# Performance work log

Hardware: AMD Instinct MI355X
Metric: run time of the kernel (lower is better)

The kernel has to match this reference:

```python
import jax, jax.numpy as jnp
import numpy as np

B, C, H, W = 32, 64, 64, 64
K = 512  # n_embeddings
D = 64   # embedding_dim


def setup_inputs() -> dict:
    key = jax.random.key(0)
    k1, k2 = jax.random.split(key)
    inputs = jax.random.normal(k1, (B, C, H, W), dtype=jnp.float32)
    embedding = jax.random.normal(k2, (K, D), dtype=jnp.float32)
    weight = jnp.ones((K,), dtype=jnp.float32)
    return {"inputs": inputs, "embedding": embedding, "weight": weight}


def reference(inputs, embedding, weight):
    # NCHW -> NHWC, flatten to [N, D]
    x = jnp.transpose(inputs, (0, 2, 3, 1))  # [B,H,W,D]
    input_shape = x.shape
    flat = x.reshape(-1, D)                  # [N,D], N = B*H*W
    n = flat.shape[0]

    usage = jnp.sum(weight >= 0.01)

    # squared Euclidean distances (argmin-equivalent to torch.cdist)
    d2 = (jnp.sum(flat * flat, axis=1, keepdims=True)
          - 2.0 * (flat @ embedding.T)
          + jnp.sum(embedding * embedding, axis=1))  # [N,K]
    indices = jnp.argmin(d2, axis=1)                 # [N]

    # one-hot assignment stats (scatter -> bincount form)
    counts = jnp.zeros((K,), dtype=flat.dtype).at[indices].add(1.0)
    avg_probs = counts / n
    perplexity = jnp.exp(-jnp.sum(avg_probs * jnp.log(avg_probs + 1e-10)))

    # straight-through quantization
    q = embedding[indices].reshape(input_shape)      # [B,H,W,D]
    quantized = jax.lax.stop_gradient(q) + x - jax.lax.stop_gradient(x)

    commitment_loss = jnp.mean((jax.lax.stop_gradient(quantized) - x) ** 2)

    quantized_nchw = jnp.transpose(quantized, (0, 3, 1, 2))
    return quantized_nchw, commitment_loss, perplexity, usage, indices
```

## Files before the change

### kernel.cpp

```cpp
#include <hip/hip_runtime.h>


typedef __attribute__((ext_vector_type(8))) _Float16 f16x8;
typedef __attribute__((ext_vector_type(4))) float f32x4;
typedef unsigned int uint;
typedef unsigned short ushort;

namespace {
constexpr int kC = 64, kH = 64, kW = 64;
constexpr int kK = 512, kD = 64;
constexpr int kHW = kH * kW;
constexpr int kCHW = kC * kHW;
constexpr int kN = 32 * kHW;
constexpr int kQElems = 32 * kC * kHW;
constexpr uint kGapFP = 21u;
}

__device__ __forceinline__ ushort hb(_Float16 h) { return __builtin_bit_cast(ushort, h); }
__device__ __forceinline__ uint umin(uint a, uint b) { return a < b ? a : b; }
__device__ __forceinline__ uint umax(uint a, uint b) { return a > b ? a : b; }

__device__ __forceinline__ void gld16(const void* g, void* l) {
  __builtin_amdgcn_global_load_lds(
      (const __attribute__((address_space(1))) uint*)g,
      (__attribute__((address_space(3))) uint*)l, 16, 0, 0);
}

__global__ __launch_bounds__(64) void vq_prep(const float* __restrict__ emb,
                                              ushort* __restrict__ embPh,
                                              ushort* __restrict__ embPl,
                                              float* __restrict__ embT,
                                              float* __restrict__ enorm,
                                              uint* __restrict__ counts,
                                              uint* __restrict__ flag_count) {
  const int k = blockIdx.x * 64 + threadIdx.x;
  const float4* __restrict__ ep4 = (const float4*)(emb + k * kD);
  float ev[kD];
  uint uh[32], ul[32];
  float s = 0.f;
#pragma unroll
  for (int j = 0; j < kD / 4; ++j) {
    const float4 v = ep4[j];
    ev[4 * j] = v.x; ev[4 * j + 1] = v.y; ev[4 * j + 2] = v.z; ev[4 * j + 3] = v.w;
    s = fmaf(v.x, v.x, s); s = fmaf(v.y, v.y, s);
    s = fmaf(v.z, v.z, s); s = fmaf(v.w, v.w, s);
#pragma unroll
    for (int t = 0; t < 2; ++t) {
      const float e0 = ev[4 * j + 2 * t] * 2048.f;
      const float e1 = ev[4 * j + 2 * t + 1] * 2048.f;
      const _Float16 h0 = (_Float16)e0, h1 = (_Float16)e1;
      const _Float16 l0 = (_Float16)(e0 - (float)h0);
      const _Float16 l1 = (_Float16)(e1 - (float)h1);
      uh[2 * j + t] = (uint)hb(h0) | ((uint)hb(h1) << 16);
      ul[2 * j + t] = (uint)hb(l0) | ((uint)hb(l1) << 16);
    }
  }
  uint4* __restrict__ ph4 = (uint4*)embPh;
  uint4* __restrict__ pl4 = (uint4*)embPl;
#pragma unroll
  for (int cc = 0; cc < 8; ++cc) {
    const int dst = k * 8 + (cc ^ (k & 7));
    ph4[dst] = uint4{uh[4 * cc], uh[4 * cc + 1], uh[4 * cc + 2], uh[4 * cc + 3]};
    pl4[dst] = uint4{ul[4 * cc], ul[4 * cc + 1], ul[4 * cc + 2], ul[4 * cc + 3]};
  }
#pragma unroll
  for (int c = 0; c < kD; ++c) embT[c * kK + k] = ev[c];
  enorm[k] = s;
  counts[k] = 0u;
  if (k == 0) *flag_count = 0u;
}

__global__ __launch_bounds__(512, 4) void vq_assign(
    const float* __restrict__ in, const ushort* __restrict__ embPh,
    const ushort* __restrict__ embPl, const float* __restrict__ embT,
    const float* __restrict__ enorm, float* __restrict__ idx_out,
    float* __restrict__ outq, uint* __restrict__ counts,
    float* __restrict__ partial, uint* __restrict__ flag_count,
    uint* __restrict__ flags, uint flag_cap) {
  __shared__ __align__(16) ushort xbh[128 * 64];
  __shared__ __align__(16) ushort xbl[128 * 64];
  __shared__ __align__(16) ushort ebh[2][4096];
  __shared__ __align__(16) ushort ebl[2][4096];
  __shared__ uint mm1[4][128], mm2[4][128];
  __shared__ float xnp[4][128];
  __shared__ uint hist[512];
  __shared__ uint fidx[128];

  const int tid = threadIdx.x;
  const int lane = tid & 63;
  const int wv = __builtin_amdgcn_readfirstlane(tid >> 6);
  const int ph = wv >> 2;
  const int cs = wv & 3;
  const int c = lane & 15;
  const int g = lane >> 4;

  const int blk = blockIdx.x;
  const int bb = blk >> 5;
  const int hw0 = (blk & 31) << 7;
  const float* __restrict__ xp = in + (size_t)bb * kCHW + hw0 + ph * 64;

  hist[tid] = 0u;

  auto stageE = [&](int buf, int st) {
    const size_t src = (size_t)st * 8192 + cs * 2048;
    const int dst = cs * 2048;
#pragma unroll
    for (int i = 0; i < 2; ++i) {
      gld16((const char*)embPh + src + i * 1024 + lane * 16,
            (char*)&ebh[buf][0] + dst + i * 1024);
      gld16((const char*)embPl + src + i * 1024 + lane * 16,
            (char*)&ebl[buf][0] + dst + i * 1024);
    }
  };
  stageE(0, 0);

  float en_pre[8];
#pragma unroll
  for (int st = 0; st < 8; ++st)
    en_pre[st] = (enorm[st * 64 + cs * 16 + c] + 256.f) * 2048.f;

  {
    const int p = lane;
    uint uh[8], ul[8];
    float xn = 0.f;
#pragma unroll
    for (int j = 0; j < 8; ++j) {
      const float f0 = xp[(size_t)(cs * 16 + 2 * j) * kHW + p];
      const float f1 = xp[(size_t)(cs * 16 + 2 * j + 1) * kHW + p];
      xn = fmaf(f0, f0, xn);
      xn = fmaf(f1, f1, xn);
      const float m0 = -2.f * f0, m1f = -2.f * f1;
      const _Float16 h0 = (_Float16)m0, h1 = (_Float16)m1f;
      const _Float16 l0 = (_Float16)(m0 - (float)h0);
      const _Float16 l1 = (_Float16)(m1f - (float)h1);
      uh[j] = (uint)hb(h0) | ((uint)hb(h1) << 16);
      ul[j] = (uint)hb(l0) | ((uint)hb(l1) << 16);
    }
    const int row = ph * 64 + p;
    const int swz = (row & 7) << 4;
    const int o0 = (row * 128 + cs * 32) ^ swz;
    const int o1 = (row * 128 + cs * 32 + 16) ^ swz;
    *(uint4*)((char*)xbh + o0) = uint4{uh[0], uh[1], uh[2], uh[3]};
    *(uint4*)((char*)xbh + o1) = uint4{uh[4], uh[5], uh[6], uh[7]};
    *(uint4*)((char*)xbl + o0) = uint4{ul[0], ul[1], ul[2], ul[3]};
    *(uint4*)((char*)xbl + o1) = uint4{ul[4], ul[5], ul[6], ul[7]};
    xnp[cs][row] = xn;
  }
  __syncthreads();

  uint m1[16], m2[16];
#pragma unroll
  for (int i = 0; i < 16; ++i) { m1[i] = 0xFFFFFFFFu; m2[i] = 0xFFFFFFFFu; }

#pragma unroll
  for (int st = 0; st < 8; ++st) {
    if (st < 7) stageE((st & 1) ^ 1, st + 1);

    if (st < 7) {
      asm volatile("s_waitcnt vmcnt(4)" ::: "memory");
    } else {
      asm volatile("s_waitcnt vmcnt(0)" ::: "memory");
    }
    __builtin_amdgcn_sched_barrier(0);

    const int rowb = cs * 16 + c;
    const int swb = (rowb & 7) << 4;
    const int ob0 = (rowb * 128 + g * 16) ^ swb;
    const int ob1 = (rowb * 128 + g * 16 + 64) ^ swb;
    const int bsel = st & 1;
    const f16x8 bh0 = *(const f16x8*)((const char*)&ebh[bsel][0] + ob0);
    const f16x8 bh1 = *(const f16x8*)((const char*)&ebh[bsel][0] + ob1);
    const f16x8 bl0 = *(const f16x8*)((const char*)&ebl[bsel][0] + ob0);
    const f16x8 bl1 = *(const f16x8*)((const char*)&ebl[bsel][0] + ob1);
    const float en = en_pre[st];
    const uint kor = (uint)(st * 64 + cs * 16 + c);
    __builtin_amdgcn_s_setprio(1);
#pragma unroll
    for (int rt = 0; rt < 4; ++rt) {
      f16x8 ah[2], al[2];
#pragma unroll
      for (int s = 0; s < 2; ++s) {
        const int row = ph * 64 + rt * 16 + c;
        const int off = (row * 128 + g * 16 + s * 64) ^ ((row & 7) << 4);
        ah[s] = *(const f16x8*)((const char*)xbh + off);
        al[s] = *(const f16x8*)((const char*)xbl + off);
      }
      f32x4 acc0 = {en, en, en, en};
      f32x4 acc1 = {0.f, 0.f, 0.f, 0.f};
      acc0 = __builtin_amdgcn_mfma_f32_16x16x32_f16(ah[0], bh0, acc0, 0, 0, 0);
      acc1 = __builtin_amdgcn_mfma_f32_16x16x32_f16(ah[1], bh1, acc1, 0, 0, 0);
      acc0 = __builtin_amdgcn_mfma_f32_16x16x32_f16(ah[0], bl0, acc0, 0, 0, 0);
      acc1 = __builtin_amdgcn_mfma_f32_16x16x32_f16(ah[1], bl1, acc1, 0, 0, 0);
      acc0 = __builtin_amdgcn_mfma_f32_16x16x32_f16(al[0], bh0, acc0, 0, 0, 0);
      acc1 = __builtin_amdgcn_mfma_f32_16x16x32_f16(al[1], bh1, acc1, 0, 0, 0);
#pragma unroll
      for (int r = 0; r < 4; ++r) {
        const uint u = ((uint)(acc0[r] + acc1[r]) << 9) | kor;
        const int i = rt * 4 + r;
        const uint t = umax(m1[i], u);
        m1[i] = umin(m1[i], u);
        m2[i] = umin(m2[i], t);
      }
    }
    __builtin_amdgcn_s_setprio(0);

    asm volatile("s_waitcnt lgkmcnt(0)" ::: "memory");
    __builtin_amdgcn_sched_barrier(0);
    __builtin_amdgcn_s_barrier();
  }

#pragma unroll
  for (int i = 0; i < 16; ++i) {
    uint a1 = m1[i], a2 = m2[i];
#pragma unroll
    for (int off = 1; off < 16; off <<= 1) {
      const uint o1 = __shfl_xor(a1, off, 64);
      const uint o2 = __shfl_xor(a2, off, 64);
      const uint t = umax(a1, o1);
      a1 = umin(a1, o1);
      a2 = umin(umin(a2, o2), t);
    }
    m1[i] = a1; m2[i] = a2;
  }

  if (c == 0) {
#pragma unroll
    for (int i = 0; i < 16; ++i) {
      const int p = ph * 64 + (i >> 2) * 16 + g * 4 + (i & 3);
      mm1[cs][p] = m1[i];
      mm2[cs][p] = m2[i];
    }
  }
  __syncthreads();

  if (tid < 128) {
    uint a1 = mm1[0][tid], a2 = mm2[0][tid];
#pragma unroll
    for (int s = 1; s < 4; ++s) {
      const uint u1 = mm1[s][tid], u2 = mm2[s][tid];
      const uint t = umax(a1, u1);
      a1 = umin(a1, u1);
      a2 = umin(umin(a2, u2), t);
    }
    const uint bidx = a1 & 511u;
    fidx[tid] = bidx;
    idx_out[blk * 128 + tid] = (float)bidx;
    if (((a2 >> 9) - (a1 >> 9)) < kGapFP) {
      const uint slot = atomicAdd(flag_count, 1u);
      if (slot < flag_cap) flags[slot] = (uint)(blk * 128 + tid);
    }
    atomicAdd(&hist[bidx], 1u);

    const float xnorm = (xnp[0][tid] + xnp[1][tid]) + (xnp[2][tid] + xnp[3][tid]);
    float d2 = fmaf((float)(a1 >> 9), 1.f / 2048.f, -256.f) + xnorm;
#pragma unroll
    for (int off = 32; off > 0; off >>= 1) d2 += __shfl_down(d2, off, 64);
    if ((tid & 63) == 0) partial[blk * 2 + (tid >> 6)] = d2;
  }
  __syncthreads();
  if (hist[tid]) atomicAdd(&counts[tid], hist[tid]);

  {
    const int ch = tid >> 3;
    const int wq = tid & 7;
    const float* __restrict__ tr = embT + ch * kK;
    float* __restrict__ oq = outq + (size_t)bb * kCHW + (size_t)ch * kHW + hw0 + wq * 16;
#pragma unroll
    for (int i = 0; i < 4; ++i) {
      const int p0 = wq * 16 + i * 4;
      float4 v;
      v.x = tr[fidx[p0 + 0]];
      v.y = tr[fidx[p0 + 1]];
      v.z = tr[fidx[p0 + 2]];
      v.w = tr[fidx[p0 + 3]];
      *(float4*)(oq + i * 4) = v;
    }
  }
}

__global__ __launch_bounds__(256) void vq_refine(const float* __restrict__ in,
                                                 const float* __restrict__ emb,
                                                 const uint* __restrict__ flag_count,
                                                 const uint* __restrict__ flags,
                                                 uint flag_cap,
                                                 float* __restrict__ idx_out,
                                                 float* __restrict__ outq) {
  uint cnt = *flag_count;
  if (cnt > flag_cap) cnt = flag_cap;
  const int lane = threadIdx.x & 63;
  const uint wave_id = blockIdx.x * 4u + (threadIdx.x >> 6);
  const uint wave_stride = gridDim.x * 4u;

  for (uint i = wave_id; i < cnt; i += wave_stride) {
    const int n = (int)flags[i];
    const int b = n >> 12;
    const int hw = n & 4095;
    const float* __restrict__ xp = in + (size_t)b * kCHW + hw;

    float xr[kD];
#pragma unroll
    for (int d = 0; d < kD; ++d) xr[d] = xp[(size_t)d * kHW];

    double best = 1e300;
    int bidx = 0;
#pragma unroll 1
    for (int kk = 0; kk < 8; ++kk) {
      const int k = lane * 8 + kk;
      const float4* __restrict__ ep4 = (const float4*)(emb + k * kD);
      double s0 = 0.0, s1 = 0.0;
#pragma unroll
      for (int j = 0; j < kD / 4; ++j) {
        const float4 e = ep4[j];
        const double d0 = (double)xr[4 * j + 0] - (double)e.x;
        const double d1 = (double)xr[4 * j + 1] - (double)e.y;
        const double d2 = (double)xr[4 * j + 2] - (double)e.z;
        const double d3 = (double)xr[4 * j + 3] - (double)e.w;
        s0 = fma(d0, d0, s0);
        s1 = fma(d1, d1, s1);
        s0 = fma(d2, d2, s0);
        s1 = fma(d3, d3, s1);
      }
      const double s = s0 + s1;
      if (s < best) { best = s; bidx = k; }
    }
#pragma unroll
    for (int off = 32; off > 0; off >>= 1) {
      const double ob = __shfl_xor(best, off, 64);
      const int oi = __shfl_xor(bidx, off, 64);
      if (ob < best || (ob == best && oi < bidx)) { best = ob; bidx = oi; }
    }
    if (lane == 0) idx_out[n] = (float)bidx;
    outq[(size_t)b * kCHW + (size_t)lane * kHW + hw] = emb[bidx * kD + lane];
  }
}

__global__ __launch_bounds__(512) void vq_finalize(const float* __restrict__ weight,
                                                   const uint* __restrict__ counts,
                                                   const float* __restrict__ partial,
                                                   float* __restrict__ out_scalars) {
  __shared__ float red[512];
  const int t = threadIdx.x;

  const float avg = (float)counts[t] / (float)kN;
  red[t] = avg * logf(avg + 1e-10f);
  __syncthreads();
#pragma unroll
  for (int off = 256; off > 0; off >>= 1) {
    if (t < off) red[t] += red[t + off];
    __syncthreads();
  }
  const float perp = expf(-red[0]);
  __syncthreads();

  red[t] = (partial[t] + partial[t + 512]) + (partial[t + 1024] + partial[t + 1536]);
  __syncthreads();
#pragma unroll
  for (int off = 256; off > 0; off >>= 1) {
    if (t < off) red[t] += red[t + off];
    __syncthreads();
  }
  const float loss = red[0] / (float)((long long)kN * (long long)kD);
  __syncthreads();

  red[t] = (weight[t] >= 0.01f) ? 1.f : 0.f;
  __syncthreads();
#pragma unroll
  for (int off = 256; off > 0; off >>= 1) {
    if (t < off) red[t] += red[t + off];
    __syncthreads();
  }
  if (t == 0) {
    out_scalars[0] = loss;
    out_scalars[1] = perp;
    out_scalars[2] = red[0];
  }
}

extern "C" void kernel_launch(void* const* d_in, const int* in_sizes, int n_in,
                              void* d_out, int out_size, void* d_ws, size_t ws_size,
                              hipStream_t stream) {
  const float* in = (const float*)d_in[0];
  const float* emb = (const float*)d_in[1];
  const float* weight = (const float*)d_in[2];
  float* out = (float*)d_out;

  float* ws_f = (float*)d_ws;
  uint* ws_u = (uint*)d_ws;
  ushort* embPh = (ushort*)d_ws;
  ushort* embPl = embPh + kK * kD;
  float* embT = ws_f + 32768;
  float* enorm = ws_f + 65536;
  uint* counts = ws_u + 66048;
  float* partial = ws_f + 66560;
  uint* flag_count = ws_u + 68608;
  uint* flags = ws_u + 68609;
  const size_t ws_elems = ws_size / 4;
  const uint flag_cap =
      (ws_elems > 68609)
          ? (uint)((ws_elems - 68609 < (size_t)kN) ? ws_elems - 68609 : (size_t)kN)
          : 0u;

  float* outq = out;
  float* out_scalars = out + kQElems;
  float* idx_out = out + kQElems + 3;

  vq_prep<<<8, 64, 0, stream>>>(emb, embPh, embPl, embT, enorm, counts, flag_count);
  vq_assign<<<kN / 128, 512, 0, stream>>>(in, embPh, embPl, embT, enorm, idx_out,
                                          outq, counts, partial, flag_count, flags,
                                          flag_cap);
  vq_refine<<<256, 256, 0, stream>>>(in, emb, flag_count, flags, flag_cap,
                                     idx_out, outq);
  vq_finalize<<<1, 512, 0, stream>>>(weight, counts, partial, out_scalars);
}
```

Measured before the change: 91.37 us.

## Gather codebook rows into LDS for the quantized-output transpose instead of the transposed table

Drops the transposed codebook copy (embT) from the prep kernel. The assign kernel now gathers the selected codebook rows from the original row-major embedding with coalesced float4 loads into a swizzled LDS tile, then reads them back transposed to write the NCHW output. The goal is to replace scattered per-element global gathers with contiguous row loads and to remove the strided embT writes in prep. In exchange it adds an extra LDS pass and barrier, and it reuses the x staging area for the tile, which grows the LDS carve-out to a single 74 KB buffer that could affect occupancy.

```diff
diff --git a/kernel.cpp b/kernel.cpp
--- a/kernel.cpp
+++ b/kernel.cpp
@@ -29,31 +29,30 @@
 __global__ __launch_bounds__(64) void vq_prep(const float* __restrict__ emb,
                                               ushort* __restrict__ embPh,
                                               ushort* __restrict__ embPl,
-                                              float* __restrict__ embT,
                                               float* __restrict__ enorm,
                                               uint* __restrict__ counts,
                                               uint* __restrict__ flag_count) {
   const int k = blockIdx.x * 64 + threadIdx.x;
   const float4* __restrict__ ep4 = (const float4*)(emb + k * kD);
-  float ev[kD];
   uint uh[32], ul[32];
   float s = 0.f;
 #pragma unroll
   for (int j = 0; j < kD / 4; ++j) {
     const float4 v = ep4[j];
-    ev[4 * j] = v.x; ev[4 * j + 1] = v.y; ev[4 * j + 2] = v.z; ev[4 * j + 3] = v.w;
     s = fmaf(v.x, v.x, s); s = fmaf(v.y, v.y, s);
     s = fmaf(v.z, v.z, s); s = fmaf(v.w, v.w, s);
-#pragma unroll
-    for (int t = 0; t < 2; ++t) {
-      const float e0 = ev[4 * j + 2 * t] * 2048.f;
-      const float e1 = ev[4 * j + 2 * t + 1] * 2048.f;
-      const _Float16 h0 = (_Float16)e0, h1 = (_Float16)e1;
-      const _Float16 l0 = (_Float16)(e0 - (float)h0);
-      const _Float16 l1 = (_Float16)(e1 - (float)h1);
-      uh[2 * j + t] = (uint)hb(h0) | ((uint)hb(h1) << 16);
-      ul[2 * j + t] = (uint)hb(l0) | ((uint)hb(l1) << 16);
-    }
+    const float e0 = v.x * 2048.f, e1 = v.y * 2048.f;
+    const float e2 = v.z * 2048.f, e3 = v.w * 2048.f;
+    const _Float16 h0 = (_Float16)e0, h1 = (_Float16)e1;
+    const _Float16 h2 = (_Float16)e2, h3 = (_Float16)e3;
+    const _Float16 l0 = (_Float16)(e0 - (float)h0);
+    const _Float16 l1 = (_Float16)(e1 - (float)h1);
+    const _Float16 l2 = (_Float16)(e2 - (float)h2);
+    const _Float16 l3 = (_Float16)(e3 - (float)h3);
+    uh[2 * j] = (uint)hb(h0) | ((uint)hb(h1) << 16);
+    uh[2 * j + 1] = (uint)hb(h2) | ((uint)hb(h3) << 16);
+    ul[2 * j] = (uint)hb(l0) | ((uint)hb(l1) << 16);
+    ul[2 * j + 1] = (uint)hb(l2) | ((uint)hb(l3) << 16);
   }
   uint4* __restrict__ ph4 = (uint4*)embPh;
   uint4* __restrict__ pl4 = (uint4*)embPl;
@@ -63,28 +62,29 @@
     ph4[dst] = uint4{uh[4 * cc], uh[4 * cc + 1], uh[4 * cc + 2], uh[4 * cc + 3]};
     pl4[dst] = uint4{ul[4 * cc], ul[4 * cc + 1], ul[4 * cc + 2], ul[4 * cc + 3]};
   }
-#pragma unroll
-  for (int c = 0; c < kD; ++c) embT[c * kK + k] = ev[c];
   enorm[k] = s;
   counts[k] = 0u;
   if (k == 0) *flag_count = 0u;
 }
 
 __global__ __launch_bounds__(512, 4) void vq_assign(
-    const float* __restrict__ in, const ushort* __restrict__ embPh,
-    const ushort* __restrict__ embPl, const float* __restrict__ embT,
+    const float* __restrict__ in, const float* __restrict__ emb,
+    const ushort* __restrict__ embPh, const ushort* __restrict__ embPl,
     const float* __restrict__ enorm, float* __restrict__ idx_out,
     float* __restrict__ outq, uint* __restrict__ counts,
     float* __restrict__ partial, uint* __restrict__ flag_count,
     uint* __restrict__ flags, uint flag_cap) {
-  __shared__ __align__(16) ushort xbh[128 * 64];
-  __shared__ __align__(16) ushort xbl[128 * 64];
-  __shared__ __align__(16) ushort ebh[2][4096];
-  __shared__ __align__(16) ushort ebl[2][4096];
-  __shared__ uint mm1[4][128], mm2[4][128];
-  __shared__ float xnp[4][128];
-  __shared__ uint hist[512];
-  __shared__ uint fidx[128];
+  __shared__ __align__(16) char lds[74240];
+  char* __restrict__ xbh = lds;
+  char* __restrict__ xbl = lds + 16384;
+  char* __restrict__ ebh = lds + 32768;
+  char* __restrict__ ebl = lds + 49152;
+  uint* __restrict__ mm1 = (uint*)(lds + 65536);
+  uint* __restrict__ mm2 = (uint*)(lds + 67584);
+  float* __restrict__ xnp = (float*)(lds + 69632);
+  uint* __restrict__ hist = (uint*)(lds + 71680);
+  uint* __restrict__ fidx = (uint*)(lds + 73728);
+  float* __restrict__ ldsE = (float*)lds;
 
   const int tid = threadIdx.x;
   const int lane = tid & 63;
@@ -103,13 +103,11 @@
 
   auto stageE = [&](int buf, int st) {
     const size_t src = (size_t)st * 8192 + cs * 2048;
-    const int dst = cs * 2048;
+    const int dst = buf * 8192 + cs * 2048;
 #pragma unroll
     for (int i = 0; i < 2; ++i) {
-      gld16((const char*)embPh + src + i * 1024 + lane * 16,
-            (char*)&ebh[buf][0] + dst + i * 1024);
-      gld16((const char*)embPl + src + i * 1024 + lane * 16,
-            (char*)&ebl[buf][0] + dst + i * 1024);
+      gld16((const char*)embPh + src + i * 1024 + lane * 16, ebh + dst + i * 1024);
+      gld16((const char*)embPl + src + i * 1024 + lane * 16, ebl + dst + i * 1024);
     }
   };
   stageE(0, 0);
@@ -140,11 +138,11 @@
     const int swz = (row & 7) << 4;
     const int o0 = (row * 128 + cs * 32) ^ swz;
     const int o1 = (row * 128 + cs * 32 + 16) ^ swz;
-    *(uint4*)((char*)xbh + o0) = uint4{uh[0], uh[1], uh[2], uh[3]};
-    *(uint4*)((char*)xbh + o1) = uint4{uh[4], uh[5], uh[6], uh[7]};
-    *(uint4*)((char*)xbl + o0) = uint4{ul[0], ul[1], ul[2], ul[3]};
-    *(uint4*)((char*)xbl + o1) = uint4{ul[4], ul[5], ul[6], ul[7]};
-    xnp[cs][row] = xn;
+    *(uint4*)(xbh + o0) = uint4{uh[0], uh[1], uh[2], uh[3]};
+    *(uint4*)(xbh + o1) = uint4{uh[4], uh[5], uh[6], uh[7]};
+    *(uint4*)(xbl + o0) = uint4{ul[0], ul[1], ul[2], ul[3]};
+    *(uint4*)(xbl + o1) = uint4{ul[4], ul[5], ul[6], ul[7]};
+    xnp[cs * 128 + row] = xn;
   }
   __syncthreads();
 
@@ -165,13 +163,13 @@
 
     const int rowb = cs * 16 + c;
     const int swb = (rowb & 7) << 4;
-    const int ob0 = (rowb * 128 + g * 16) ^ swb;
-    const int ob1 = (rowb * 128 + g * 16 + 64) ^ swb;
-    const int bsel = st & 1;
-    const f16x8 bh0 = *(const f16x8*)((const char*)&ebh[bsel][0] + ob0);
-    const f16x8 bh1 = *(const f16x8*)((const char*)&ebh[bsel][0] + ob1);
-    const f16x8 bl0 = *(const f16x8*)((const char*)&ebl[bsel][0] + ob0);
-    const f16x8 bl1 = *(const f16x8*)((const char*)&ebl[bsel][0] + ob1);
+    const int bbase = (st & 1) * 8192;
+    const int ob0 = bbase + ((rowb * 128 + g * 16) ^ swb);
+    const int ob1 = bbase + ((rowb * 128 + g * 16 + 64) ^ swb);
+    const f16x8 bh0 = *(const f16x8*)(ebh + ob0);
+    const f16x8 bh1 = *(const f16x8*)(ebh + ob1);
+    const f16x8 bl0 = *(const f16x8*)(ebl + ob0);
+    const f16x8 bl1 = *(const f16x8*)(ebl + ob1);
     const float en = en_pre[st];
     const uint kor = (uint)(st * 64 + cs * 16 + c);
     __builtin_amdgcn_s_setprio(1);
@@ -182,8 +180,8 @@
       for (int s = 0; s < 2; ++s) {
         const int row = ph * 64 + rt * 16 + c;
         const int off = (row * 128 + g * 16 + s * 64) ^ ((row & 7) << 4);
-        ah[s] = *(const f16x8*)((const char*)xbh + off);
-        al[s] = *(const f16x8*)((const char*)xbl + off);
+        ah[s] = *(const f16x8*)(xbh + off);
+        al[s] = *(const f16x8*)(xbl + off);
       }
       f32x4 acc0 = {en, en, en, en};
       f32x4 acc1 = {0.f, 0.f, 0.f, 0.f};
@@ -227,17 +225,17 @@
 #pragma unroll
     for (int i = 0; i < 16; ++i) {
       const int p = ph * 64 + (i >> 2) * 16 + g * 4 + (i & 3);
-      mm1[cs][p] = m1[i];
-      mm2[cs][p] = m2[i];
+      mm1[cs * 128 + p] = m1[i];
+      mm2[cs * 128 + p] = m2[i];
     }
   }
   __syncthreads();
 
   if (tid < 128) {
-    uint a1 = mm1[0][tid], a2 = mm2[0][tid];
+    uint a1 = mm1[tid], a2 = mm2[tid];
 #pragma unroll
     for (int s = 1; s < 4; ++s) {
-      const uint u1 = mm1[s][tid], u2 = mm2[s][tid];
+      const uint u1 = mm1[s * 128 + tid], u2 = mm2[s * 128 + tid];
       const uint t = umax(a1, u1);
       a1 = umin(a1, u1);
       a2 = umin(umin(a2, u2), t);
@@ -251,7 +249,7 @@
     }
     atomicAdd(&hist[bidx], 1u);
 
-    const float xnorm = (xnp[0][tid] + xnp[1][tid]) + (xnp[2][tid] + xnp[3][tid]);
+    const float xnorm = (xnp[tid] + xnp[128 + tid]) + (xnp[256 + tid] + xnp[384 + tid]);
     float d2 = fmaf((float)(a1 >> 9), 1.f / 2048.f, -256.f) + xnorm;
 #pragma unroll
     for (int off = 32; off > 0; off >>= 1) d2 += __shfl_down(d2, off, 64);
@@ -260,21 +258,28 @@
   __syncthreads();
   if (hist[tid]) atomicAdd(&counts[tid], hist[tid]);
 
+#pragma unroll
+  for (int pass = 0; pass < 4; ++pass) {
+    const int r = pass * 32 + (tid >> 4);
+    const int q = tid & 15;
+    const float4 v = *(const float4*)(emb + fidx[r] * kD + q * 4);
+    const int cswz = (q * 4) ^ (((r >> 4) & 7) << 3);
+    *(float4*)(ldsE + r * 64 + cswz) = v;
+  }
+  __syncthreads();
   {
     const int ch = tid >> 3;
     const int wq = tid & 7;
-    const float* __restrict__ tr = embT + ch * kK;
     float* __restrict__ oq = outq + (size_t)bb * kCHW + (size_t)ch * kHW + hw0 + wq * 16;
-#pragma unroll
-    for (int i = 0; i < 4; ++i) {
-      const int p0 = wq * 16 + i * 4;
-      float4 v;
-      v.x = tr[fidx[p0 + 0]];
-      v.y = tr[fidx[p0 + 1]];
-      v.z = tr[fidx[p0 + 2]];
-      v.w = tr[fidx[p0 + 3]];
-      *(float4*)(oq + i * 4) = v;
-    }
+    float4 vv[4];
+#pragma unroll
+    for (int i = 0; i < 16; ++i) {
+      const int p = wq * 16 + i;
+      const int cswz = ch ^ (((p >> 4) & 7) << 3);
+      ((float*)vv)[i] = ldsE[p * 64 + cswz];
+    }
+#pragma unroll
+    for (int i = 0; i < 4; ++i) *(float4*)(oq + i * 4) = vv[i];
   }
 }
 
@@ -388,7 +393,6 @@
   uint* ws_u = (uint*)d_ws;
   ushort* embPh = (ushort*)d_ws;
   ushort* embPl = embPh + kK * kD;
-  float* embT = ws_f + 32768;
   float* enorm = ws_f + 65536;
   uint* counts = ws_u + 66048;
   float* partial = ws_f + 66560;
@@ -404,8 +408,8 @@
   float* out_scalars = out + kQElems;
   float* idx_out = out + kQElems + 3;
 
-  vq_prep<<<8, 64, 0, stream>>>(emb, embPh, embPl, embT, enorm, counts, flag_count);
-  vq_assign<<<kN / 128, 512, 0, stream>>>(in, embPh, embPl, embT, enorm, idx_out,
+  vq_prep<<<8, 64, 0, stream>>>(emb, embPh, embPl, enorm, counts, flag_count);
+  vq_assign<<<kN / 128, 512, 0, stream>>>(in, emb, embPh, embPl, enorm, idx_out,
                                           outq, counts, partial, flag_count, flags,
                                           flag_cap);
   vq_refine<<<256, 256, 0, stream>>>(in, emb, flag_count, flags, flag_cap,
```

After: 87.85 us. -3.9%, faster.
